# Optimization experiments

Measured on AMD Instinct MI355X. Metric: run time of the kernel, lower is better.

Reference implementation:

```python
import jax, jax.numpy as jnp
import numpy as np

B, T, V, E, U = 64, 256, 32000, 512, 1024


def setup_inputs() -> dict:
    key = jax.random.key(0)
    k1, k2, k3 = jax.random.split(key, 3)
    tokens = jax.random.randint(k1, (B, T), 0, V)
    hidden = jnp.zeros((B, U), dtype=jnp.float32)
    emb = jax.random.normal(k2, (V, E), dtype=jnp.float32) * 0.05
    kx, kh = jax.random.split(k3)
    # Keras GRU v2: kernel [E, 3U], recurrent_kernel [U, 3U], reset_after=True -> two bias vectors
    Wx = jax.random.normal(kx, (E, 3 * U), dtype=jnp.float32) * 0.02
    bx = jnp.zeros((3 * U,), dtype=jnp.float32)
    Wh = jax.random.normal(kh, (U, 3 * U), dtype=jnp.float32) * 0.02
    bh = jnp.zeros((3 * U,), dtype=jnp.float32)
    return {"tokens": tokens, "hidden": hidden, "emb": emb,
            "Wx": Wx, "bx": bx, "Wh": Wh, "bh": bh}


def _gru_scan(x_proj, h0, Wh, bh, units):
    # x_proj: [T, B, 3U] precomputed input projections (incl. input bias)
    def step(h, xt):
        rec = h @ Wh + bh                      # [B, 3U]
        xz, xr, xh = jnp.split(xt, 3, axis=-1)
        hz, hr, hh = jnp.split(rec, 3, axis=-1)
        z = jax.nn.sigmoid(xz + hz)
        r = jax.nn.sigmoid(xr + hr)
        cand = jnp.tanh(xh + r * hh)           # reset_after=True: r applied after matmul
        h_new = z * h + (1.0 - z) * cand
        return h_new, h_new
    h_last, seq = jax.lax.scan(step, h0, x_proj)
    return seq, h_last


def reference(tokens, hidden, emb, Wx, bx, Wh, bh):
    x = emb[tokens]                            # [B, T, E] embedding lookup
    x_proj = jnp.einsum('bte,eu->btu', x, Wx) + bx  # [B, T, 3U]
    seq, h_last = _gru_scan(jnp.swapaxes(x_proj, 0, 1), hidden, Wh, bh, U)
    output = jnp.swapaxes(seq, 0, 1)           # [B, T, U]
    return output, h_last
```

## Files before the change

kernel.cpp:

```cpp
#include <hip/hip_runtime.h>
#include <cstdint>

typedef _Float16 f16x8 __attribute__((ext_vector_type(8)));
typedef float    f32x4 __attribute__((ext_vector_type(4)));
typedef unsigned int u32;

#define BB 64
#define TT 256
#define EE 512
#define UU 1024
#define NN 3072

__global__ __launch_bounds__(256) void prep_whf(const float* __restrict__ Wh,
                                                _Float16* __restrict__ WhF) {
    int tid  = blockIdx.x * 256 + threadIdx.x;
    int col8 = tid % 384;
    int k    = tid / 384;
    int kb = k >> 5, quad = (k >> 3) & 3, jj = k & 7;
    const float* src = Wh + (long)k * NN + col8 * 8;
#pragma unroll
    for (int i = 0; i < 8; i++) {
        int n   = col8 * 8 + i;
        int g   = n >> 10;
        int nl  = n & 1023;
        int j   = nl >> 4, l16 = nl & 15;
        int lane = quad * 16 + l16;
        WhF[((((j * 3 + g) * 32 + kb) * 64 + lane) << 3) + jj] = (_Float16)src[i];
    }
}

__global__ __launch_bounds__(256) void prep_h0(const float* __restrict__ h0,
                                               _Float16* __restrict__ hbuf) {
    int i = blockIdx.x * 256 + threadIdx.x;
    hbuf[i] = (_Float16)h0[i];
}

__global__ __launch_bounds__(256) void proj_kernel(
    const int* __restrict__ tokens, const float* __restrict__ emb,
    const float* __restrict__ Wx, const float* __restrict__ bx,
    _Float16* __restrict__ xproj) {
    int tid  = threadIdx.x;
    int wave = tid >> 6, lane = tid & 63, quad = lane >> 4, l16 = lane & 15;
    int bm = blockIdx.x * 64;
    int bn = blockIdx.y * 128;
    int wm = (wave & 1) * 32, wn = (wave >> 1) * 64;

    int row0 = bm + wm + l16;
    const float* a0p = emb + (long)tokens[row0] * EE;
    const float* a1p = emb + (long)tokens[row0 + 16] * EE;

    f32x4 acc[2][4];
#pragma unroll
    for (int mt = 0; mt < 2; mt++)
#pragma unroll
        for (int nt = 0; nt < 4; nt++) { f32x4 z = {0.f, 0.f, 0.f, 0.f}; acc[mt][nt] = z; }

#pragma unroll 2
    for (int k0 = 0; k0 < EE; k0 += 32) {
        int ka = k0 + quad * 8;
        f16x8 afr[2];
        {
            const float4* p = (const float4*)(a0p + ka);
            float4 x0 = p[0], x1 = p[1];
            afr[0][0] = (_Float16)x0.x; afr[0][1] = (_Float16)x0.y;
            afr[0][2] = (_Float16)x0.z; afr[0][3] = (_Float16)x0.w;
            afr[0][4] = (_Float16)x1.x; afr[0][5] = (_Float16)x1.y;
            afr[0][6] = (_Float16)x1.z; afr[0][7] = (_Float16)x1.w;
        }
        {
            const float4* p = (const float4*)(a1p + ka);
            float4 x0 = p[0], x1 = p[1];
            afr[1][0] = (_Float16)x0.x; afr[1][1] = (_Float16)x0.y;
            afr[1][2] = (_Float16)x0.z; afr[1][3] = (_Float16)x0.w;
            afr[1][4] = (_Float16)x1.x; afr[1][5] = (_Float16)x1.y;
            afr[1][6] = (_Float16)x1.z; afr[1][7] = (_Float16)x1.w;
        }
        f16x8 bfr[4];
#pragma unroll
        for (int nt = 0; nt < 4; nt++) {
            const float* bp = Wx + (long)ka * NN + (bn + wn + nt * 16 + l16);
#pragma unroll
            for (int jj = 0; jj < 8; jj++) bfr[nt][jj] = (_Float16)bp[(long)jj * NN];
        }
#pragma unroll
        for (int mt = 0; mt < 2; mt++)
#pragma unroll
            for (int nt = 0; nt < 4; nt++)
                acc[mt][nt] = __builtin_amdgcn_mfma_f32_16x16x32_f16(afr[mt], bfr[nt], acc[mt][nt], 0, 0, 0);
    }
#pragma unroll
    for (int mt = 0; mt < 2; mt++) {
        int rowbase = bm + wm + mt * 16 + quad * 4;
#pragma unroll
        for (int nt = 0; nt < 4; nt++) {
            int col = bn + wn + nt * 16 + l16;
            float bias = bx[col];
#pragma unroll
            for (int r = 0; r < 4; r++) {
                int i = rowbase + r;
                int b = i >> 8, t = i & 255;
                xproj[((long)t * BB + b) * NN + col] = (_Float16)(acc[mt][nt][r] + bias);
            }
        }
    }
}

__global__ __launch_bounds__(256, 1) void gru_kernel(
    const _Float16* __restrict__ xproj,
    const _Float16* __restrict__ WhF,
    const float* __restrict__ hidden,
    const float* __restrict__ bh,
    _Float16* __restrict__ hbuf,
    u32* cnt,
    float* __restrict__ out) {
    int tid  = threadIdx.x;
    int wave = tid >> 6, lane = tid & 63, quad = lane >> 4, l16 = lane & 15;
    int j  = blockIdx.x;
    int u  = j * 16 + l16;
    int b0 = wave * 16;

    float bhz = bh[u], bhr = bh[UU + u], bhh = bh[2 * UU + u];

    float hold[4];
#pragma unroll
    for (int r = 0; r < 4; r++) hold[r] = hidden[(long)(b0 + quad * 4 + r) * UU + u];

    const f16x8* WF = (const f16x8*)WhF + (long)j * 3 * 32 * 64 + lane;
    f16x8 w[96];
#pragma unroll
    for (int i = 0; i < 96; i++) w[i] = WF[(long)i * 64];
#pragma unroll
    for (int i = 0; i < 60; i++) asm volatile("" : "+a"(w[i]));
#pragma unroll
    for (int i = 60; i < 96; i++) asm volatile("" : "+v"(w[i]));

#pragma unroll 1
    for (int t = 0; t < TT; t++) {
        const _Float16* xp = xproj + (long)t * BB * NN;
        float xzv[4], xrv[4], xhv[4];
#pragma unroll
        for (int r = 0; r < 4; r++) {
            const _Float16* p = xp + (long)(b0 + quad * 4 + r) * NN + u;
            xzv[r] = (float)p[0]; xrv[r] = (float)p[UU]; xhv[r] = (float)p[2 * UU];
        }

        const _Float16* h = hbuf + (long)(t & 1) * BB * UU + (long)(b0 + l16) * UU + quad * 8;
        f32x4 az = {0.f, 0.f, 0.f, 0.f}, ar = az, ah = az;
#pragma unroll
        for (int kb = 0; kb < 32; kb++) {
            f16x8 afr = *(const f16x8*)(h + kb * 32);
            az = __builtin_amdgcn_mfma_f32_16x16x32_f16(afr, w[kb],      az, 0, 0, 0);
            ar = __builtin_amdgcn_mfma_f32_16x16x32_f16(afr, w[32 + kb], ar, 0, 0, 0);
            ah = __builtin_amdgcn_mfma_f32_16x16x32_f16(afr, w[64 + kb], ah, 0, 0, 0);
        }

        _Float16* hw = hbuf + (long)((t + 1) & 1) * BB * UU;
#pragma unroll
        for (int r = 0; r < 4; r++) {
            int b = b0 + quad * 4 + r;
            float z  = 1.f / (1.f + expf(-(xzv[r] + az[r] + bhz)));
            float rr = 1.f / (1.f + expf(-(xrv[r] + ar[r] + bhr)));
            float cd = tanhf(xhv[r] + rr * (ah[r] + bhh));
            float hn = z * hold[r] + (1.f - z) * cd;
            hold[r] = hn;
            out[(long)b * TT * UU + (long)t * UU + u] = hn;
            u32 hv = (u32)__builtin_bit_cast(unsigned short, (_Float16)hn);
            asm volatile("global_store_short %0, %1, off sc0 sc1"
                         :: "v"(hw + (long)b * UU + u), "v"(hv) : "memory");
        }

        if (t != TT - 1) {
            __syncthreads();
            if (tid == 0) {
                __hip_atomic_fetch_add(cnt + (j >> 3) * 16, 1u,
                                       __ATOMIC_RELAXED, __HIP_MEMORY_SCOPE_AGENT);
                u32 tgt = 8u * (u32)(t + 1);
                for (;;) {
                    u32 c0, c1, c2, c3, c4, c5, c6, c7;
                    asm volatile(
                        "global_load_dword %0, %8, off sc0 sc1\n\t"
                        "global_load_dword %1, %8, off offset:64 sc0 sc1\n\t"
                        "global_load_dword %2, %8, off offset:128 sc0 sc1\n\t"
                        "global_load_dword %3, %8, off offset:192 sc0 sc1\n\t"
                        "global_load_dword %4, %8, off offset:256 sc0 sc1\n\t"
                        "global_load_dword %5, %8, off offset:320 sc0 sc1\n\t"
                        "global_load_dword %6, %8, off offset:384 sc0 sc1\n\t"
                        "global_load_dword %7, %8, off offset:448 sc0 sc1\n\t"
                        "s_waitcnt vmcnt(0)"
                        : "=&v"(c0), "=&v"(c1), "=&v"(c2), "=&v"(c3),
                          "=&v"(c4), "=&v"(c5), "=&v"(c6), "=&v"(c7)
                        : "v"(cnt) : "memory");
                    if (c0 >= tgt && c1 >= tgt && c2 >= tgt && c3 >= tgt &&
                        c4 >= tgt && c5 >= tgt && c6 >= tgt && c7 >= tgt) break;
                    __builtin_amdgcn_s_sleep(1);
                }
                __builtin_amdgcn_fence(__ATOMIC_ACQUIRE, "agent");
            }
            __syncthreads();
        }
    }
#pragma unroll
    for (int r = 0; r < 4; r++) {
        int b = b0 + quad * 4 + r;
        out[(long)BB * TT * UU + (long)b * UU + u] = hold[r];
    }
}

extern "C" void kernel_launch(void* const* d_in, const int* in_sizes, int n_in,
                              void* d_out, int out_size, void* d_ws, size_t ws_size,
                              hipStream_t stream) {
    const int*   tokens = (const int*)d_in[0];
    const float* hidden = (const float*)d_in[1];
    const float* emb    = (const float*)d_in[2];
    const float* Wx     = (const float*)d_in[3];
    const float* bx     = (const float*)d_in[4];
    const float* Wh     = (const float*)d_in[5];
    const float* bh     = (const float*)d_in[6];
    float* out = (float*)d_out;

    char* ws = (char*)d_ws;
    _Float16* xproj = (_Float16*)(ws);
    _Float16* WhF   = (_Float16*)(ws + 100663296L);
    _Float16* hbuf  = (_Float16*)(ws + 106954752L);
    u32*      cnt   = (u32*)(ws + 107216896L);
    if (ws_size < 107217408UL) return;

    hipMemsetAsync(cnt, 0, 512, stream);
    prep_whf<<<1536, 256, 0, stream>>>(Wh, WhF);
    prep_h0<<<256, 256, 0, stream>>>(hidden, hbuf);
    proj_kernel<<<dim3(256, 24), 256, 0, stream>>>(tokens, emb, Wx, bx, xproj);
    gru_kernel<<<64, 256, 0, stream>>>(xproj, WhF, hidden, bh, hbuf, cnt, out);
}
```

Before: 2.580 ms.

## Software-pipeline hidden-state loads with MFMA in persistent GRU recurrence

Replaces the compiler-scheduled per-iteration f16x8 loads of the previous hidden state with explicit uncached global_load_dwordx4 into a 16-deep ring. Loads are issued ahead and waited on in groups with manual vmcnt, so memory latency overlaps the MFMA chain of each timestep. It also moves four more weight fragments into AGPRs and drops the acquire fence after the spin-wait, relying on sc0 sc1 loads for coherence. Manual waitcnt assumes no other outstanding vector memory ops, and removing the fence risks memory-ordering issues.

Result: faster. 2.487 ms (-3.6%).

```diff
diff --git a/kernel.cpp b/kernel.cpp
--- a/kernel.cpp
+++ b/kernel.cpp
@@ -10,6 +10,8 @@
 #define EE 512
 #define UU 1024
 #define NN 3072
+
+#define MFMA16(a, b, c) __builtin_amdgcn_mfma_f32_16x16x32_f16((a), (b), (c), 0, 0, 0)
 
 __global__ __launch_bounds__(256) void prep_whf(const float* __restrict__ Wh,
                                                 _Float16* __restrict__ WhF) {
@@ -86,7 +88,7 @@
         for (int mt = 0; mt < 2; mt++)
 #pragma unroll
             for (int nt = 0; nt < 4; nt++)
-                acc[mt][nt] = __builtin_amdgcn_mfma_f32_16x16x32_f16(afr[mt], bfr[nt], acc[mt][nt], 0, 0, 0);
+                acc[mt][nt] = MFMA16(afr[mt], bfr[nt], acc[mt][nt]);
     }
 #pragma unroll
     for (int mt = 0; mt < 2; mt++) {
@@ -130,9 +132,9 @@
 #pragma unroll
     for (int i = 0; i < 96; i++) w[i] = WF[(long)i * 64];
 #pragma unroll
-    for (int i = 0; i < 60; i++) asm volatile("" : "+a"(w[i]));
-#pragma unroll
-    for (int i = 60; i < 96; i++) asm volatile("" : "+v"(w[i]));
+    for (int i = 0; i < 64; i++) asm volatile("" : "+a"(w[i]));
+#pragma unroll
+    for (int i = 64; i < 96; i++) asm volatile("" : "+v"(w[i]));
 
 #pragma unroll 1
     for (int t = 0; t < TT; t++) {
@@ -144,14 +146,36 @@
             xzv[r] = (float)p[0]; xrv[r] = (float)p[UU]; xhv[r] = (float)p[2 * UU];
         }
 
-        const _Float16* h = hbuf + (long)(t & 1) * BB * UU + (long)(b0 + l16) * UU + quad * 8;
+        const _Float16* h = hbuf + (long)(t & 1) * BB * UU
+                                 + (long)(b0 + l16) * UU + quad * 8;
+        f16x8 hf[16];
+#pragma unroll
+        for (int kb = 0; kb < 16; kb++)
+            asm volatile("global_load_dwordx4 %0, %1, off sc0 sc1"
+                         : "=v"(hf[kb]) : "v"(h + (long)kb * 32));
+
         f32x4 az = {0.f, 0.f, 0.f, 0.f}, ar = az, ah = az;
 #pragma unroll
-        for (int kb = 0; kb < 32; kb++) {
-            f16x8 afr = *(const f16x8*)(h + kb * 32);
-            az = __builtin_amdgcn_mfma_f32_16x16x32_f16(afr, w[kb],      az, 0, 0, 0);
-            ar = __builtin_amdgcn_mfma_f32_16x16x32_f16(afr, w[32 + kb], ar, 0, 0, 0);
-            ah = __builtin_amdgcn_mfma_f32_16x16x32_f16(afr, w[64 + kb], ah, 0, 0, 0);
+        for (int q = 0; q < 4; q++) {
+            if (q < 3) asm volatile("s_waitcnt vmcnt(8)" ::: "memory");
+            else       asm volatile("s_waitcnt vmcnt(0)" ::: "memory");
+            __builtin_amdgcn_sched_barrier(0);
+#pragma unroll
+            for (int i = 0; i < 8; i++) {
+                int kb = q * 8 + i;
+                f16x8 afr = hf[kb & 15];
+                az = MFMA16(afr, w[kb],      az);
+                ar = MFMA16(afr, w[32 + kb], ar);
+                ah = MFMA16(afr, w[64 + kb], ah);
+            }
+            if (q < 2) {
+#pragma unroll
+                for (int i = 0; i < 8; i++) {
+                    int kb2 = 16 + q * 8 + i;
+                    asm volatile("global_load_dwordx4 %0, %1, off sc0 sc1"
+                                 : "=v"(hf[kb2 & 15]) : "v"(h + (long)kb2 * 32));
+                }
+            }
         }
 
         _Float16* hw = hbuf + (long)((t + 1) & 1) * BB * UU;
@@ -194,7 +218,6 @@
                         c4 >= tgt && c5 >= tgt && c6 >= tgt && c7 >= tgt) break;
                     __builtin_amdgcn_s_sleep(1);
                 }
-                __builtin_amdgcn_fence(__ATOMIC_ACQUIRE, "agent");
             }
             __syncthreads();
         }
```
